# Kernel optimization log

Hardware: AMD Instinct MI355X
Metric: run time of the kernel (lower is better)

## Reference

```python
import jax, jax.numpy as jnp
import numpy as np

RES = 256
RADIUS = 1.3
N_INTRS = 128
STEP = 2.0 * RADIUS / N_INTRS
GRID_DIM = 2
RANK = 8


def bilinear_sample(grid, coords):
    """grid: [C,H,W]; coords: [N,2] in [-1,1] (x->W, y->H), align_corners=True, border clamp."""
    C, H, W = grid.shape
    x = jnp.clip((coords[:, 0] + 1.0) * 0.5 * (W - 1), 0.0, W - 1)
    y = jnp.clip((coords[:, 1] + 1.0) * 0.5 * (H - 1), 0.0, H - 1)
    x0 = jnp.clip(jnp.floor(x), 0, W - 2).astype(jnp.int32)
    y0 = jnp.clip(jnp.floor(y), 0, H - 2).astype(jnp.int32)
    x1, y1 = x0 + 1, y0 + 1
    wx = x - x0
    wy = y - y0
    g00 = grid[:, y0, x0]  # [C,N]
    g01 = grid[:, y0, x1]
    g10 = grid[:, y1, x0]
    g11 = grid[:, y1, x1]
    out = (g00 * (1 - wx) * (1 - wy) + g01 * wx * (1 - wy)
           + g10 * (1 - wx) * wy + g11 * wx * wy)
    return out.T  # [N,C]


def sh_deg4(d):
    """Spherical harmonics degree 4 (16 coeffs), d: [N,3] unit dirs."""
    x, y, z = d[:, 0], d[:, 1], d[:, 2]
    xx, yy, zz = x * x, y * y, z * z
    xy, yz, xz = x * y, y * z, x * z
    return jnp.stack([
        jnp.full_like(x, 0.28209479177387814),
        -0.48860251190291987 * y,
        0.48860251190291987 * z,
        -0.48860251190291987 * x,
        1.0925484305920792 * xy,
        -1.0925484305920792 * yz,
        0.94617469575755997 * zz - 0.31539156525251999,
        -1.0925484305920792 * xz,
        0.54627421529603959 * (xx - yy),
        0.59004358992664352 * y * (-3.0 * xx + yy),
        2.8906114426405538 * xy * z,
        0.45704579946446572 * y * (1.0 - 5.0 * zz),
        0.3731763325901154 * z * (5.0 * zz - 3.0),
        0.45704579946446572 * x * (1.0 - 5.0 * zz),
        1.445305721320277 * z * (xx - yy),
        0.59004358992664352 * x * (-xx + 3.0 * yy),
    ], axis=-1)  # [N,16]


def setup_inputs() -> dict:
    key = jax.random.key(0)
    ks = jax.random.split(key, 9)
    B = 16384
    # ray origins inside the sphere so every ray hits; random unit directions
    rays_o = jax.random.normal(ks[0], (B, 3), jnp.float32) * 0.3
    rays_d = jax.random.normal(ks[1], (B, 3), jnp.float32)
    G = jax.random.normal(ks[2], (3, GRID_DIM * RANK, RES, RES), jnp.float32) * 0.1
    Fgrid = jax.random.normal(ks[3], (32, 64, 64), jnp.float32) * 0.05
    sigma_W1 = jax.random.normal(ks[4], (32, 64), jnp.float32) * (1.0 / np.sqrt(32))
    sigma_W2 = jax.random.normal(ks[5], (64, 16), jnp.float32) * (1.0 / np.sqrt(64))
    color_W1 = jax.random.normal(ks[6], (31, 64), jnp.float32) * (1.0 / np.sqrt(31))
    color_W2 = jax.random.normal(ks[7], (64, 64), jnp.float32) * (1.0 / np.sqrt(64))
    color_W3 = jax.random.normal(ks[8], (64, 3), jnp.float32) * (1.0 / np.sqrt(64))
    return {"rays_o": rays_o, "rays_d": rays_d, "G": G, "Fgrid": Fgrid,
            "sigma_W1": sigma_W1, "sigma_W2": sigma_W2,
            "color_W1": color_W1, "color_W2": color_W2, "color_W3": color_W3}


def reference(rays_o, rays_d, G, Fgrid, sigma_W1, sigma_W2, color_W1, color_W2, color_W3):
    B = rays_o.shape[0]
    d = rays_d / jnp.linalg.norm(rays_d, axis=-1, keepdims=True)
    # ray-sphere intersection (|o + t d| = RADIUS), d unit
    b = jnp.sum(rays_o * d, axis=-1)
    c = jnp.sum(rays_o * rays_o, axis=-1) - RADIUS ** 2
    disc = b * b - c
    sq = jnp.sqrt(jnp.maximum(disc, 0.0))
    near = jnp.maximum(-b - sq, 0.0)
    far = -b + sq
    ts = near[:, None] + jnp.arange(N_INTRS + 1, dtype=jnp.float32) * STEP  # [B, n+1]
    tmid = 0.5 * (ts[:, :-1] + ts[:, 1:])  # [B, n]
    mask = (disc > 0)[:, None] & (tmid <= far[:, None])  # [B, n]
    pts = rays_o[:, None, :] + d[:, None, :] * tmid[..., None]  # [B, n, 3]
    # combined rescale: ((pts/R + 1)*RES/2) * 2/RES - 1 = pts / RADIUS
    p = (pts / RADIUS).reshape(-1, 3)  # [N, 3] in ~[-1,1]
    # tri-plane sampling
    coo = jnp.stack([p[:, [0, 1]], p[:, [0, 2]], p[:, [1, 2]]])  # [3, N, 2]
    interp = jax.vmap(bilinear_sample)(G, coo)  # [3, N, GRID_DIM*RANK]
    interp = interp.reshape(3, -1, GRID_DIM, RANK)
    Gvals = interp.prod(axis=0).sum(axis=-1)  # [N, GRID_DIM]
    Fvals = bilinear_sample(Fgrid, Gvals)  # [N, feature_dim]
    h = jax.nn.relu(Fvals @ sigma_W1) @ sigma_W2  # [N, 16]
    sigma_pts = h[:, 0]
    feat = h[:, 1:]
    rd = jnp.broadcast_to(d[:, None, :], (B, N_INTRS, 3)).reshape(-1, 3)
    enc = sh_deg4(rd)  # [N, 16]
    cin = jnp.concatenate([enc, feat], axis=-1)  # [N, 31]
    col = jax.nn.relu(jax.nn.relu(cin @ color_W1) @ color_W2) @ color_W3  # [N, 3]
    mflat = mask.reshape(-1)
    sigma = jax.nn.relu(jnp.where(mflat, sigma_pts, 0.0)).reshape(B, N_INTRS)
    color = jnp.where(mflat[:, None], col, 0.0).reshape(B, N_INTRS, 3)
    # sigma2alpha + compositing (white background)
    delta = ts[:, 1:] - ts[:, :-1]
    alpha = 1.0 - jnp.exp(-sigma * delta)
    trans = jnp.cumprod(1.0 - alpha + 1e-10, axis=1)
    T = jnp.concatenate([jnp.ones_like(trans[:, :1]), trans[:, :-1]], axis=1)
    w = alpha * T  # [B, n]
    rgb = jax.nn.sigmoid(color)
    acc = jnp.sum(w, axis=1)
    out = jnp.einsum('bn,bnc->bc', w, rgb) + (1.0 - acc)[:, None]
    return out
```

## Files before the change

kernel.cpp:

```cpp
#include <hip/hip_runtime.h>
#include <math.h>

#define B_RAYS 16384
#define N_I 128
constexpr float RADIUS_ = 1.3f;
constexpr float STEP_ = 0.0203125f;

typedef float v2f __attribute__((ext_vector_type(2)));
static __device__ __forceinline__ v2f mk2(float a, float b) { v2f r; r.x = a; r.y = b; return r; }
static __device__ __forceinline__ v2f vfma(v2f a, v2f b, v2f c) {
    return __builtin_elementwise_fma(a, b, c);
}

__global__ __launch_bounds__(256) void k_transposeG(const float* __restrict__ G,
                                                    float* __restrict__ Gt) {
    int pl = blockIdx.x >> 8;
    int y  = blockIdx.x & 255;
    __shared__ float tile[16][257];
    int t = threadIdx.x;
#pragma unroll
    for (int ch = 0; ch < 16; ++ch)
        tile[ch][t] = G[((pl * 16 + ch) * 256 + y) * 256 + t];
    __syncthreads();
    float* dst = Gt + (pl * 256 + y) * 256 * 16;
#pragma unroll
    for (int i = 0; i < 16; ++i) {
        int o = i * 256 + t;
        dst[o] = tile[o & 15][o >> 4];
    }
}

__global__ __launch_bounds__(256) void k_transposeF(const float* __restrict__ F,
                                                    float* __restrict__ Ft) {
    int y = blockIdx.x;
    __shared__ float tile[32][65];
    int t = threadIdx.x;
#pragma unroll
    for (int i = 0; i < 8; ++i) {
        int o = i * 256 + t;
        tile[o >> 6][o & 63] = F[((o >> 6) * 64 + y) * 64 + (o & 63)];
    }
    __syncthreads();
    float* dst = Ft + y * 64 * 32;
#pragma unroll
    for (int i = 0; i < 8; ++i) {
        int o = i * 256 + t;
        dst[o] = tile[o & 31][o >> 5];
    }
}

__global__ __launch_bounds__(256) void k_fused(
    const float* __restrict__ rays_o, const float* __restrict__ rays_d,
    const float* __restrict__ Gt, const float* __restrict__ Ft,
    const float* __restrict__ sW1, const float* __restrict__ sW2,
    const float* __restrict__ cW1, const float* __restrict__ cW2,
    const float* __restrict__ cW3, float* __restrict__ out) {
    __shared__ float w_s1t[64 * 32];
    __shared__ float w_s2[64 * 16];
    __shared__ float w_c1t[64 * 32];
    __shared__ float w_c2[64 * 64];
    __shared__ float w_c3[64 * 3];
    int tid = threadIdx.x;
    for (int i = tid; i < 2048; i += 256) { float v = sW1[i]; w_s1t[(i & 63) * 32 + (i >> 6)] = v; }
    for (int i = tid; i < 1024; i += 256) w_s2[i] = sW2[i];
    for (int i = tid; i < 1984; i += 256) { float v = cW1[i]; w_c1t[(i & 63) * 32 + (i >> 6)] = v; }
    for (int i = tid; i < 64; i += 256) w_c1t[i * 32 + 31] = 0.f;
    for (int i = tid; i < 4096; i += 256) w_c2[i] = cW2[i];
    if (tid < 192) w_c3[tid] = cW3[tid];
    __syncthreads();

    int lane = tid & 63;
    int ray  = (blockIdx.x << 2) + (tid >> 6);

    float ox = rays_o[ray * 3 + 0], oy = rays_o[ray * 3 + 1], oz = rays_o[ray * 3 + 2];
    float rx = rays_d[ray * 3 + 0], ry = rays_d[ray * 3 + 1], rz = rays_d[ray * 3 + 2];
    float nrm = sqrtf(rx * rx + ry * ry + rz * rz);
    float dx = rx / nrm, dy = ry / nrm, dz = rz / nrm;
    float bq = ox * dx + oy * dy + oz * dz;
    float cq = ox * ox + oy * oy + oz * oz - RADIUS_ * RADIUS_;
    float disc = bq * bq - cq;
    float sq = sqrtf(fmaxf(disc, 0.f));
    float tnear = fmaxf(-bq - sq, 0.f);
    float tfar = -bq + sq;

    v2f e[8];
    {
        float x = dx, y = dy, z = dz;
        float xx = x * x, yy = y * y, zz = z * z;
        float xy = x * y, yz = y * z, xz = x * z;
        e[0] = mk2(0.28209479177387814f, -0.48860251190291987f * y);
        e[1] = mk2(0.48860251190291987f * z, -0.48860251190291987f * x);
        e[2] = mk2(1.0925484305920792f * xy, -1.0925484305920792f * yz);
        e[3] = mk2(0.94617469575756f * zz - 0.31539156525252f, -1.0925484305920792f * xz);
        e[4] = mk2(0.5462742152960396f * (xx - yy),
                   0.5900435899266435f * y * (-3.0f * xx + yy));
        e[5] = mk2(2.890611442640554f * xy * z,
                   0.4570457994644657f * y * (1.0f - 5.0f * zz));
        e[6] = mk2(0.3731763325901154f * z * (5.0f * zz - 3.0f),
                   0.4570457994644657f * x * (1.0f - 5.0f * zz));
        e[7] = mk2(1.445305721320277f * z * (xx - yy),
                   0.5900435899266435f * x * (-xx + 3.0f * yy));
    }

    float4 res[2];
#pragma unroll
    for (int u = 0; u < 2; ++u) {
        int s = (lane << 1) + u;
        float t0 = tnear + (float)s * STEP_;
        float t1 = tnear + (float)(s + 1) * STEP_;
        float tmid = 0.5f * (t0 + t1);
        bool mask = (disc > 0.f) && (tmid <= tfar);
        if (!mask) {
            res[u] = make_float4(0.f, 0.f, 0.f, 0.f);
        } else {
            float px = (ox + dx * tmid) / RADIUS_;
            float py = (oy + dy * tmid) / RADIUS_;
            float pz = (oz + dz * tmid) / RADIUS_;

            v2f pr[8];
            float cxs[3] = {px, px, py};
            float cys[3] = {py, pz, pz};
#pragma unroll
            for (int pl = 0; pl < 3; ++pl) {
                float fx = fminf(fmaxf((cxs[pl] + 1.0f) * 0.5f * 255.0f, 0.f), 255.f);
                float fy = fminf(fmaxf((cys[pl] + 1.0f) * 0.5f * 255.0f, 0.f), 255.f);
                float x0f = fminf(floorf(fx), 254.f);
                float y0f = fminf(floorf(fy), 254.f);
                int x0 = (int)x0f, y0 = (int)y0f;
                float wx = fx - x0f, wy = fy - y0f;
                v2f w00 = mk2((1.f - wx) * (1.f - wy), (1.f - wx) * (1.f - wy));
                v2f w01 = mk2(wx * (1.f - wy), wx * (1.f - wy));
                v2f w10 = mk2((1.f - wx) * wy, (1.f - wx) * wy);
                v2f w11 = mk2(wx * wy, wx * wy);
                const float* b00 = Gt + ((pl * 256 + y0) * 256 + x0) * 16;
#pragma unroll
                for (int q = 0; q < 4; ++q) {
                    float4 g00 = *(const float4*)(b00 + q * 4);
                    float4 g01 = *(const float4*)(b00 + 16 + q * 4);
                    float4 g10 = *(const float4*)(b00 + 4096 + q * 4);
                    float4 g11 = *(const float4*)(b00 + 4112 + q * 4);
                    v2f lo = mk2(g00.x, g00.y) * w00;
                    lo = vfma(mk2(g01.x, g01.y), w01, lo);
                    lo = vfma(mk2(g10.x, g10.y), w10, lo);
                    lo = vfma(mk2(g11.x, g11.y), w11, lo);
                    v2f hi = mk2(g00.z, g00.w) * w00;
                    hi = vfma(mk2(g01.z, g01.w), w01, hi);
                    hi = vfma(mk2(g10.z, g10.w), w10, hi);
                    hi = vfma(mk2(g11.z, g11.w), w11, hi);
                    if (pl == 0) { pr[2 * q] = lo; pr[2 * q + 1] = hi; }
                    else         { pr[2 * q] *= lo; pr[2 * q + 1] *= hi; }
                }
            }
            v2f sx = (pr[0] + pr[1]) + (pr[2] + pr[3]);
            v2f sy = (pr[4] + pr[5]) + (pr[6] + pr[7]);
            float Gx = sx.x + sx.y;
            float Gy = sy.x + sy.y;

            v2f fv[16];
            {
                float fx = fminf(fmaxf((Gx + 1.0f) * 0.5f * 63.0f, 0.f), 63.f);
                float fy = fminf(fmaxf((Gy + 1.0f) * 0.5f * 63.0f, 0.f), 63.f);
                float x0f = fminf(floorf(fx), 62.f);
                float y0f = fminf(floorf(fy), 62.f);
                int x0 = (int)x0f, y0 = (int)y0f;
                float wx = fx - x0f, wy = fy - y0f;
                v2f w00 = mk2((1.f - wx) * (1.f - wy), (1.f - wx) * (1.f - wy));
                v2f w01 = mk2(wx * (1.f - wy), wx * (1.f - wy));
                v2f w10 = mk2((1.f - wx) * wy, (1.f - wx) * wy);
                v2f w11 = mk2(wx * wy, wx * wy);
                const float* f00 = Ft + (y0 * 64 + x0) * 32;
#pragma unroll
                for (int q = 0; q < 8; ++q) {
                    float4 g00 = *(const float4*)(f00 + q * 4);
                    float4 g01 = *(const float4*)(f00 + 32 + q * 4);
                    float4 g10 = *(const float4*)(f00 + 2048 + q * 4);
                    float4 g11 = *(const float4*)(f00 + 2048 + 32 + q * 4);
                    v2f lo = mk2(g00.x, g00.y) * w00;
                    lo = vfma(mk2(g01.x, g01.y), w01, lo);
                    lo = vfma(mk2(g10.x, g10.y), w10, lo);
                    lo = vfma(mk2(g11.x, g11.y), w11, lo);
                    v2f hi = mk2(g00.z, g00.w) * w00;
                    hi = vfma(mk2(g01.z, g01.w), w01, hi);
                    hi = vfma(mk2(g10.z, g10.w), w10, hi);
                    hi = vfma(mk2(g11.z, g11.w), w11, hi);
                    fv[2 * q] = lo;
                    fv[2 * q + 1] = hi;
                }
            }

            v2f hh2[8];
#pragma unroll
            for (int m = 0; m < 8; ++m) hh2[m] = mk2(0.f, 0.f);
            for (int j = 0; j < 64; ++j) {
                const float4* wrow = (const float4*)&w_s1t[j * 32];
                v2f aA = mk2(0.f, 0.f), aB = mk2(0.f, 0.f);
#pragma unroll
                for (int q = 0; q < 8; ++q) {
                    float4 w = wrow[q];
                    aA = vfma(fv[2 * q], mk2(w.x, w.y), aA);
                    aB = vfma(fv[2 * q + 1], mk2(w.z, w.w), aB);
                }
                v2f asum = aA + aB;
                float a = fmaxf(asum.x + asum.y, 0.f);
                v2f av = mk2(a, a);
                const float4* w2row = (const float4*)&w_s2[j * 16];
#pragma unroll
                for (int q = 0; q < 4; ++q) {
                    float4 w = w2row[q];
                    hh2[2 * q] = vfma(av, mk2(w.x, w.y), hh2[2 * q]);
                    hh2[2 * q + 1] = vfma(av, mk2(w.z, w.w), hh2[2 * q + 1]);
                }
            }

            v2f cf[8];
            cf[0] = mk2(hh2[0].y, hh2[1].x);
            cf[1] = mk2(hh2[1].y, hh2[2].x);
            cf[2] = mk2(hh2[2].y, hh2[3].x);
            cf[3] = mk2(hh2[3].y, hh2[4].x);
            cf[4] = mk2(hh2[4].y, hh2[5].x);
            cf[5] = mk2(hh2[5].y, hh2[6].x);
            cf[6] = mk2(hh2[6].y, hh2[7].x);
            cf[7] = mk2(hh2[7].y, 0.f);

            v2f c2v[32];
#pragma unroll
            for (int m = 0; m < 32; ++m) c2v[m] = mk2(0.f, 0.f);
            for (int j = 0; j < 64; ++j) {
                const float4* wrow = (const float4*)&w_c1t[j * 32];
                v2f aA = mk2(0.f, 0.f), aB = mk2(0.f, 0.f);
#pragma unroll
                for (int q = 0; q < 4; ++q) {
                    float4 w = wrow[q];
                    aA = vfma(e[2 * q], mk2(w.x, w.y), aA);
                    aB = vfma(e[2 * q + 1], mk2(w.z, w.w), aB);
                }
#pragma unroll
                for (int q = 0; q < 4; ++q) {
                    float4 w = wrow[4 + q];
                    aA = vfma(cf[2 * q], mk2(w.x, w.y), aA);
                    aB = vfma(cf[2 * q + 1], mk2(w.z, w.w), aB);
                }
                v2f asum = aA + aB;
                float a = fmaxf(asum.x + asum.y, 0.f);
                v2f av = mk2(a, a);
                const float4* w2row = (const float4*)&w_c2[j * 64];
#pragma unroll
                for (int q = 0; q < 16; ++q) {
                    float4 w = w2row[q];
                    c2v[2 * q] = vfma(av, mk2(w.x, w.y), c2v[2 * q]);
                    c2v[2 * q + 1] = vfma(av, mk2(w.z, w.w), c2v[2 * q + 1]);
                }
            }
            v2f col01 = mk2(0.f, 0.f);
            float col2 = 0.f;
#pragma unroll
            for (int m = 0; m < 64; ++m) {
                float v = fmaxf((m & 1) ? c2v[m >> 1].y : c2v[m >> 1].x, 0.f);
                col01 = vfma(mk2(v, v), mk2(w_c3[m * 3 + 0], w_c3[m * 3 + 1]), col01);
                col2 = fmaf(v, w_c3[m * 3 + 2], col2);
            }

            float sigma = fmaxf(hh2[0].x, 0.f);
            float r = 1.f / (1.f + expf(-col01.x));
            float g = 1.f / (1.f + expf(-col01.y));
            float b = 1.f / (1.f + expf(-col2));
            res[u] = make_float4(sigma, r, g, b);
        }
    }

    int s0 = lane * 2;
    float4 p0 = res[0];
    float4 p1 = res[1];
    float ta = tnear + (float)s0 * STEP_;
    float tb = tnear + (float)(s0 + 1) * STEP_;
    float tc = tnear + (float)(s0 + 2) * STEP_;
    float d0 = tb - ta, d1 = tc - tb;
    float alpha0 = 1.f - expf(-p0.x * d0);
    float alpha1 = 1.f - expf(-p1.x * d1);
    float f0 = (1.f - alpha0) + 1e-10f;
    float f1 = (1.f - alpha1) + 1e-10f;
    float fp = f0 * f1;

    float P = fp;
#pragma unroll
    for (int dlt = 1; dlt < 64; dlt <<= 1) {
        float v = __shfl_up(P, dlt, 64);
        if (lane >= dlt) P *= v;
    }
    float E = __shfl_up(P, 1, 64);
    if (lane == 0) E = 1.f;

    float w0 = alpha0 * E;
    float w1 = alpha1 * (E * f0);
    float sr = w0 * p0.y + w1 * p1.y;
    float sg = w0 * p0.z + w1 * p1.z;
    float sb = w0 * p0.w + w1 * p1.w;
    float sa = w0 + w1;
#pragma unroll
    for (int m = 32; m >= 1; m >>= 1) {
        sr += __shfl_xor(sr, m, 64);
        sg += __shfl_xor(sg, m, 64);
        sb += __shfl_xor(sb, m, 64);
        sa += __shfl_xor(sa, m, 64);
    }
    if (lane == 0) {
        float bg = 1.f - sa;
        out[ray * 3 + 0] = sr + bg;
        out[ray * 3 + 1] = sg + bg;
        out[ray * 3 + 2] = sb + bg;
    }
}

extern "C" void kernel_launch(void* const* d_in, const int* in_sizes, int n_in,
                              void* d_out, int out_size, void* d_ws, size_t ws_size,
                              hipStream_t stream) {
    const float* rays_o = (const float*)d_in[0];
    const float* rays_d = (const float*)d_in[1];
    const float* G      = (const float*)d_in[2];
    const float* Fgrid  = (const float*)d_in[3];
    const float* sW1    = (const float*)d_in[4];
    const float* sW2    = (const float*)d_in[5];
    const float* cW1    = (const float*)d_in[6];
    const float* cW2    = (const float*)d_in[7];
    const float* cW3    = (const float*)d_in[8];
    float* out = (float*)d_out;

    char* ws = (char*)d_ws;
    float* Gt = (float*)ws;
    float* Ft = (float*)(ws + 12582912);

    k_transposeG<<<768, 256, 0, stream>>>(G, Gt);
    k_transposeF<<<64, 256, 0, stream>>>(Fgrid, Ft);
    k_fused<<<B_RAYS / 4, 256, 0, stream>>>(
        rays_o, rays_d, Gt, Ft, sW1, sW2, cW1, cW2, cW3, out);
}
```

Measured before the change: 824.3 us.

## Process two samples per lane jointly to share LDS weight loads

Restructures the per-lane loop so both samples of a lane run through the triplane gather, feature gather and both MLPs together, sharing each LDS weight row read across two samples. It also transposes the final color weights for float4 LDS reads and adds a waves-per-EU hint. This raises register pressure (two 64-wide accumulators at once) and may spill or lower occupancy. When sample A is active, sample B's MLP is computed and then discarded if it is masked.

After: 804.1 us. 2.4% less time.

```diff
diff --git a/kernel.cpp b/kernel.cpp
--- a/kernel.cpp
+++ b/kernel.cpp
@@ -49,7 +49,79 @@
     }
 }
 
-__global__ __launch_bounds__(256) void k_fused(
+#define FGRID_GATHER(GXQ, GYQ, FVOUT)                                              \
+    {                                                                              \
+        float fx = fminf(fmaxf(((GXQ) + 1.0f) * 0.5f * 63.0f, 0.f), 63.f);         \
+        float fy = fminf(fmaxf(((GYQ) + 1.0f) * 0.5f * 63.0f, 0.f), 63.f);         \
+        float x0f = fminf(floorf(fx), 62.f);                                       \
+        float y0f = fminf(floorf(fy), 62.f);                                       \
+        int x0 = (int)x0f, y0 = (int)y0f;                                          \
+        float wx = fx - x0f, wy = fy - y0f;                                        \
+        v2f w00 = mk2((1.f - wx) * (1.f - wy), (1.f - wx) * (1.f - wy));           \
+        v2f w01 = mk2(wx * (1.f - wy), wx * (1.f - wy));                           \
+        v2f w10 = mk2((1.f - wx) * wy, (1.f - wx) * wy);                           \
+        v2f w11 = mk2(wx * wy, wx * wy);                                           \
+        const float* f00 = Ft + (y0 * 64 + x0) * 32;                               \
+        _Pragma("unroll") for (int q = 0; q < 8; ++q) {                            \
+            float4 g00 = *(const float4*)(f00 + q * 4);                            \
+            float4 g01 = *(const float4*)(f00 + 32 + q * 4);                       \
+            float4 g10 = *(const float4*)(f00 + 2048 + q * 4);                     \
+            float4 g11 = *(const float4*)(f00 + 2048 + 32 + q * 4);                \
+            v2f lo = mk2(g00.x, g00.y) * w00;                                      \
+            lo = vfma(mk2(g01.x, g01.y), w01, lo);                                 \
+            lo = vfma(mk2(g10.x, g10.y), w10, lo);                                 \
+            lo = vfma(mk2(g11.x, g11.y), w11, lo);                                 \
+            v2f hi = mk2(g00.z, g00.w) * w00;                                      \
+            hi = vfma(mk2(g01.z, g01.w), w01, hi);                                 \
+            hi = vfma(mk2(g10.z, g10.w), w10, hi);                                 \
+            hi = vfma(mk2(g11.z, g11.w), w11, hi);                                 \
+            FVOUT[2 * q] = lo;                                                     \
+            FVOUT[2 * q + 1] = hi;                                                 \
+        }                                                                          \
+    }
+
+#define TRIPLANE(PX, PY, PZ, GXOUT, GYOUT)                                         \
+    {                                                                              \
+        v2f pr[8];                                                                 \
+        float cxs[3] = {(PX), (PX), (PY)};                                         \
+        float cys[3] = {(PY), (PZ), (PZ)};                                         \
+        _Pragma("unroll") for (int pl = 0; pl < 3; ++pl) {                         \
+            float fx = fminf(fmaxf((cxs[pl] + 1.0f) * 0.5f * 255.0f, 0.f), 255.f); \
+            float fy = fminf(fmaxf((cys[pl] + 1.0f) * 0.5f * 255.0f, 0.f), 255.f); \
+            float x0f = fminf(floorf(fx), 254.f);                                  \
+            float y0f = fminf(floorf(fy), 254.f);                                  \
+            int x0 = (int)x0f, y0 = (int)y0f;                                      \
+            float wx = fx - x0f, wy = fy - y0f;                                    \
+            v2f w00 = mk2((1.f - wx) * (1.f - wy), (1.f - wx) * (1.f - wy));       \
+            v2f w01 = mk2(wx * (1.f - wy), wx * (1.f - wy));                       \
+            v2f w10 = mk2((1.f - wx) * wy, (1.f - wx) * wy);                       \
+            v2f w11 = mk2(wx * wy, wx * wy);                                       \
+            const float* b00 = Gt + ((pl * 256 + y0) * 256 + x0) * 16;             \
+            _Pragma("unroll") for (int q = 0; q < 4; ++q) {                        \
+                float4 g00 = *(const float4*)(b00 + q * 4);                        \
+                float4 g01 = *(const float4*)(b00 + 16 + q * 4);                   \
+                float4 g10 = *(const float4*)(b00 + 4096 + q * 4);                 \
+                float4 g11 = *(const float4*)(b00 + 4112 + q * 4);                 \
+                v2f lo = mk2(g00.x, g00.y) * w00;                                  \
+                lo = vfma(mk2(g01.x, g01.y), w01, lo);                             \
+                lo = vfma(mk2(g10.x, g10.y), w10, lo);                             \
+                lo = vfma(mk2(g11.x, g11.y), w11, lo);                             \
+                v2f hi = mk2(g00.z, g00.w) * w00;                                  \
+                hi = vfma(mk2(g01.z, g01.w), w01, hi);                             \
+                hi = vfma(mk2(g10.z, g10.w), w10, hi);                             \
+                hi = vfma(mk2(g11.z, g11.w), w11, hi);                             \
+                if (pl == 0) { pr[2 * q] = lo; pr[2 * q + 1] = hi; }               \
+                else         { pr[2 * q] *= lo; pr[2 * q + 1] *= hi; }             \
+            }                                                                      \
+        }                                                                          \
+        v2f sx = (pr[0] + pr[1]) + (pr[2] + pr[3]);                                \
+        v2f sy = (pr[4] + pr[5]) + (pr[6] + pr[7]);                                \
+        GXOUT = sx.x + sx.y;                                                       \
+        GYOUT = sy.x + sy.y;                                                       \
+    }
+
+__global__ void __launch_bounds__(256)
+    __attribute__((amdgpu_waves_per_eu(2, 4))) k_fused(
     const float* __restrict__ rays_o, const float* __restrict__ rays_d,
     const float* __restrict__ Gt, const float* __restrict__ Ft,
     const float* __restrict__ sW1, const float* __restrict__ sW2,
@@ -59,14 +131,14 @@
     __shared__ float w_s2[64 * 16];
     __shared__ float w_c1t[64 * 32];
     __shared__ float w_c2[64 * 64];
-    __shared__ float w_c3[64 * 3];
+    __shared__ float w_c3t[3 * 64];
     int tid = threadIdx.x;
     for (int i = tid; i < 2048; i += 256) { float v = sW1[i]; w_s1t[(i & 63) * 32 + (i >> 6)] = v; }
     for (int i = tid; i < 1024; i += 256) w_s2[i] = sW2[i];
     for (int i = tid; i < 1984; i += 256) { float v = cW1[i]; w_c1t[(i & 63) * 32 + (i >> 6)] = v; }
     for (int i = tid; i < 64; i += 256) w_c1t[i * 32 + 31] = 0.f;
     for (int i = tid; i < 4096; i += 256) w_c2[i] = cW2[i];
-    if (tid < 192) w_c3[tid] = cW3[tid];
+    if (tid < 192) w_c3t[(tid % 3) * 64 + tid / 3] = cW3[tid];
     __syncthreads();
 
     int lane = tid & 63;
@@ -102,181 +174,172 @@
                    0.5900435899266435f * x * (-xx + 3.0f * yy));
     }
 
-    float4 res[2];
-#pragma unroll
-    for (int u = 0; u < 2; ++u) {
-        int s = (lane << 1) + u;
-        float t0 = tnear + (float)s * STEP_;
-        float t1 = tnear + (float)(s + 1) * STEP_;
-        float tmid = 0.5f * (t0 + t1);
-        bool mask = (disc > 0.f) && (tmid <= tfar);
-        if (!mask) {
-            res[u] = make_float4(0.f, 0.f, 0.f, 0.f);
-        } else {
-            float px = (ox + dx * tmid) / RADIUS_;
-            float py = (oy + dy * tmid) / RADIUS_;
-            float pz = (oz + dz * tmid) / RADIUS_;
-
-            v2f pr[8];
-            float cxs[3] = {px, px, py};
-            float cys[3] = {py, pz, pz};
-#pragma unroll
-            for (int pl = 0; pl < 3; ++pl) {
-                float fx = fminf(fmaxf((cxs[pl] + 1.0f) * 0.5f * 255.0f, 0.f), 255.f);
-                float fy = fminf(fmaxf((cys[pl] + 1.0f) * 0.5f * 255.0f, 0.f), 255.f);
-                float x0f = fminf(floorf(fx), 254.f);
-                float y0f = fminf(floorf(fy), 254.f);
-                int x0 = (int)x0f, y0 = (int)y0f;
-                float wx = fx - x0f, wy = fy - y0f;
-                v2f w00 = mk2((1.f - wx) * (1.f - wy), (1.f - wx) * (1.f - wy));
-                v2f w01 = mk2(wx * (1.f - wy), wx * (1.f - wy));
-                v2f w10 = mk2((1.f - wx) * wy, (1.f - wx) * wy);
-                v2f w11 = mk2(wx * wy, wx * wy);
-                const float* b00 = Gt + ((pl * 256 + y0) * 256 + x0) * 16;
-#pragma unroll
-                for (int q = 0; q < 4; ++q) {
-                    float4 g00 = *(const float4*)(b00 + q * 4);
-                    float4 g01 = *(const float4*)(b00 + 16 + q * 4);
-                    float4 g10 = *(const float4*)(b00 + 4096 + q * 4);
-                    float4 g11 = *(const float4*)(b00 + 4112 + q * 4);
-                    v2f lo = mk2(g00.x, g00.y) * w00;
-                    lo = vfma(mk2(g01.x, g01.y), w01, lo);
-                    lo = vfma(mk2(g10.x, g10.y), w10, lo);
-                    lo = vfma(mk2(g11.x, g11.y), w11, lo);
-                    v2f hi = mk2(g00.z, g00.w) * w00;
-                    hi = vfma(mk2(g01.z, g01.w), w01, hi);
-                    hi = vfma(mk2(g10.z, g10.w), w10, hi);
-                    hi = vfma(mk2(g11.z, g11.w), w11, hi);
-                    if (pl == 0) { pr[2 * q] = lo; pr[2 * q + 1] = hi; }
-                    else         { pr[2 * q] *= lo; pr[2 * q + 1] *= hi; }
-                }
-            }
-            v2f sx = (pr[0] + pr[1]) + (pr[2] + pr[3]);
-            v2f sy = (pr[4] + pr[5]) + (pr[6] + pr[7]);
-            float Gx = sx.x + sx.y;
-            float Gy = sy.x + sy.y;
-
-            v2f fv[16];
-            {
-                float fx = fminf(fmaxf((Gx + 1.0f) * 0.5f * 63.0f, 0.f), 63.f);
-                float fy = fminf(fmaxf((Gy + 1.0f) * 0.5f * 63.0f, 0.f), 63.f);
-                float x0f = fminf(floorf(fx), 62.f);
-                float y0f = fminf(floorf(fy), 62.f);
-                int x0 = (int)x0f, y0 = (int)y0f;
-                float wx = fx - x0f, wy = fy - y0f;
-                v2f w00 = mk2((1.f - wx) * (1.f - wy), (1.f - wx) * (1.f - wy));
-                v2f w01 = mk2(wx * (1.f - wy), wx * (1.f - wy));
-                v2f w10 = mk2((1.f - wx) * wy, (1.f - wx) * wy);
-                v2f w11 = mk2(wx * wy, wx * wy);
-                const float* f00 = Ft + (y0 * 64 + x0) * 32;
-#pragma unroll
-                for (int q = 0; q < 8; ++q) {
-                    float4 g00 = *(const float4*)(f00 + q * 4);
-                    float4 g01 = *(const float4*)(f00 + 32 + q * 4);
-                    float4 g10 = *(const float4*)(f00 + 2048 + q * 4);
-                    float4 g11 = *(const float4*)(f00 + 2048 + 32 + q * 4);
-                    v2f lo = mk2(g00.x, g00.y) * w00;
-                    lo = vfma(mk2(g01.x, g01.y), w01, lo);
-                    lo = vfma(mk2(g10.x, g10.y), w10, lo);
-                    lo = vfma(mk2(g11.x, g11.y), w11, lo);
-                    v2f hi = mk2(g00.z, g00.w) * w00;
-                    hi = vfma(mk2(g01.z, g01.w), w01, hi);
-                    hi = vfma(mk2(g10.z, g10.w), w10, hi);
-                    hi = vfma(mk2(g11.z, g11.w), w11, hi);
-                    fv[2 * q] = lo;
-                    fv[2 * q + 1] = hi;
-                }
-            }
-
-            v2f hh2[8];
-#pragma unroll
-            for (int m = 0; m < 8; ++m) hh2[m] = mk2(0.f, 0.f);
-            for (int j = 0; j < 64; ++j) {
-                const float4* wrow = (const float4*)&w_s1t[j * 32];
-                v2f aA = mk2(0.f, 0.f), aB = mk2(0.f, 0.f);
-#pragma unroll
-                for (int q = 0; q < 8; ++q) {
-                    float4 w = wrow[q];
-                    aA = vfma(fv[2 * q], mk2(w.x, w.y), aA);
-                    aB = vfma(fv[2 * q + 1], mk2(w.z, w.w), aB);
-                }
-                v2f asum = aA + aB;
-                float a = fmaxf(asum.x + asum.y, 0.f);
-                v2f av = mk2(a, a);
-                const float4* w2row = (const float4*)&w_s2[j * 16];
-#pragma unroll
-                for (int q = 0; q < 4; ++q) {
-                    float4 w = w2row[q];
-                    hh2[2 * q] = vfma(av, mk2(w.x, w.y), hh2[2 * q]);
-                    hh2[2 * q + 1] = vfma(av, mk2(w.z, w.w), hh2[2 * q + 1]);
-                }
-            }
-
-            v2f cf[8];
-            cf[0] = mk2(hh2[0].y, hh2[1].x);
-            cf[1] = mk2(hh2[1].y, hh2[2].x);
-            cf[2] = mk2(hh2[2].y, hh2[3].x);
-            cf[3] = mk2(hh2[3].y, hh2[4].x);
-            cf[4] = mk2(hh2[4].y, hh2[5].x);
-            cf[5] = mk2(hh2[5].y, hh2[6].x);
-            cf[6] = mk2(hh2[6].y, hh2[7].x);
-            cf[7] = mk2(hh2[7].y, 0.f);
-
-            v2f c2v[32];
-#pragma unroll
-            for (int m = 0; m < 32; ++m) c2v[m] = mk2(0.f, 0.f);
-            for (int j = 0; j < 64; ++j) {
-                const float4* wrow = (const float4*)&w_c1t[j * 32];
-                v2f aA = mk2(0.f, 0.f), aB = mk2(0.f, 0.f);
-#pragma unroll
-                for (int q = 0; q < 4; ++q) {
-                    float4 w = wrow[q];
-                    aA = vfma(e[2 * q], mk2(w.x, w.y), aA);
-                    aB = vfma(e[2 * q + 1], mk2(w.z, w.w), aB);
-                }
-#pragma unroll
-                for (int q = 0; q < 4; ++q) {
-                    float4 w = wrow[4 + q];
-                    aA = vfma(cf[2 * q], mk2(w.x, w.y), aA);
-                    aB = vfma(cf[2 * q + 1], mk2(w.z, w.w), aB);
-                }
-                v2f asum = aA + aB;
-                float a = fmaxf(asum.x + asum.y, 0.f);
-                v2f av = mk2(a, a);
-                const float4* w2row = (const float4*)&w_c2[j * 64];
-#pragma unroll
-                for (int q = 0; q < 16; ++q) {
-                    float4 w = w2row[q];
-                    c2v[2 * q] = vfma(av, mk2(w.x, w.y), c2v[2 * q]);
-                    c2v[2 * q + 1] = vfma(av, mk2(w.z, w.w), c2v[2 * q + 1]);
-                }
-            }
-            v2f col01 = mk2(0.f, 0.f);
-            float col2 = 0.f;
-#pragma unroll
-            for (int m = 0; m < 64; ++m) {
-                float v = fmaxf((m & 1) ? c2v[m >> 1].y : c2v[m >> 1].x, 0.f);
-                col01 = vfma(mk2(v, v), mk2(w_c3[m * 3 + 0], w_c3[m * 3 + 1]), col01);
-                col2 = fmaf(v, w_c3[m * 3 + 2], col2);
-            }
-
-            float sigma = fmaxf(hh2[0].x, 0.f);
-            float r = 1.f / (1.f + expf(-col01.x));
-            float g = 1.f / (1.f + expf(-col01.y));
-            float b = 1.f / (1.f + expf(-col2));
-            res[u] = make_float4(sigma, r, g, b);
+    int sA = lane << 1;
+    float t0A = tnear + (float)sA * STEP_;
+    float t1A = tnear + (float)(sA + 1) * STEP_;
+    float t1B = tnear + (float)(sA + 2) * STEP_;
+    float tmidA = 0.5f * (t0A + t1A);
+    float tmidB = 0.5f * (t1A + t1B);
+    bool maskA = (disc > 0.f) && (tmidA <= tfar);
+    bool maskB = (disc > 0.f) && (tmidB <= tfar);
+
+    float4 resA = make_float4(0.f, 0.f, 0.f, 0.f);
+    float4 resB = make_float4(0.f, 0.f, 0.f, 0.f);
+
+    if (maskA) {
+        float pxA = (ox + dx * tmidA) / RADIUS_;
+        float pyA = (oy + dy * tmidA) / RADIUS_;
+        float pzA = (oz + dz * tmidA) / RADIUS_;
+        float pxB = (ox + dx * tmidB) / RADIUS_;
+        float pyB = (oy + dy * tmidB) / RADIUS_;
+        float pzB = (oz + dz * tmidB) / RADIUS_;
+
+        float GxA, GyA, GxB, GyB;
+        TRIPLANE(pxA, pyA, pzA, GxA, GyA);
+        TRIPLANE(pxB, pyB, pzB, GxB, GyB);
+
+        v2f fvA[16], fvB[16];
+        FGRID_GATHER(GxA, GyA, fvA);
+        FGRID_GATHER(GxB, GyB, fvB);
+
+        v2f hhA[8], hhB[8];
+#pragma unroll
+        for (int m = 0; m < 8; ++m) { hhA[m] = mk2(0.f, 0.f); hhB[m] = mk2(0.f, 0.f); }
+        for (int j = 0; j < 64; ++j) {
+            const float4* wrow = (const float4*)&w_s1t[j * 32];
+            v2f aA0 = mk2(0.f, 0.f), aB0 = mk2(0.f, 0.f);
+            v2f aA1 = mk2(0.f, 0.f), aB1 = mk2(0.f, 0.f);
+#pragma unroll
+            for (int q = 0; q < 8; ++q) {
+                float4 w = wrow[q];
+                v2f wlo = mk2(w.x, w.y), whi = mk2(w.z, w.w);
+                aA0 = vfma(fvA[2 * q], wlo, aA0);
+                aB0 = vfma(fvA[2 * q + 1], whi, aB0);
+                aA1 = vfma(fvB[2 * q], wlo, aA1);
+                aB1 = vfma(fvB[2 * q + 1], whi, aB1);
+            }
+            v2f s0 = aA0 + aB0;
+            v2f s1 = aA1 + aB1;
+            float a0 = fmaxf(s0.x + s0.y, 0.f);
+            float a1 = fmaxf(s1.x + s1.y, 0.f);
+            v2f av0 = mk2(a0, a0), av1 = mk2(a1, a1);
+            const float4* w2row = (const float4*)&w_s2[j * 16];
+#pragma unroll
+            for (int q = 0; q < 4; ++q) {
+                float4 w = w2row[q];
+                v2f wlo = mk2(w.x, w.y), whi = mk2(w.z, w.w);
+                hhA[2 * q] = vfma(av0, wlo, hhA[2 * q]);
+                hhA[2 * q + 1] = vfma(av0, whi, hhA[2 * q + 1]);
+                hhB[2 * q] = vfma(av1, wlo, hhB[2 * q]);
+                hhB[2 * q + 1] = vfma(av1, whi, hhB[2 * q + 1]);
+            }
         }
-    }
-
-    int s0 = lane * 2;
-    float4 p0 = res[0];
-    float4 p1 = res[1];
-    float ta = tnear + (float)s0 * STEP_;
-    float tb = tnear + (float)(s0 + 1) * STEP_;
-    float tc = tnear + (float)(s0 + 2) * STEP_;
+
+        float sigmaA = fmaxf(hhA[0].x, 0.f);
+        float sigmaB = fmaxf(hhB[0].x, 0.f);
+
+        v2f cfA[8], cfB[8];
+        cfA[0] = mk2(hhA[0].y, hhA[1].x); cfB[0] = mk2(hhB[0].y, hhB[1].x);
+        cfA[1] = mk2(hhA[1].y, hhA[2].x); cfB[1] = mk2(hhB[1].y, hhB[2].x);
+        cfA[2] = mk2(hhA[2].y, hhA[3].x); cfB[2] = mk2(hhB[2].y, hhB[3].x);
+        cfA[3] = mk2(hhA[3].y, hhA[4].x); cfB[3] = mk2(hhB[3].y, hhB[4].x);
+        cfA[4] = mk2(hhA[4].y, hhA[5].x); cfB[4] = mk2(hhB[4].y, hhB[5].x);
+        cfA[5] = mk2(hhA[5].y, hhA[6].x); cfB[5] = mk2(hhB[5].y, hhB[6].x);
+        cfA[6] = mk2(hhA[6].y, hhA[7].x); cfB[6] = mk2(hhB[6].y, hhB[7].x);
+        cfA[7] = mk2(hhA[7].y, 0.f);      cfB[7] = mk2(hhB[7].y, 0.f);
+
+        v2f c2A[32], c2B[32];
+#pragma unroll
+        for (int m = 0; m < 32; ++m) { c2A[m] = mk2(0.f, 0.f); c2B[m] = mk2(0.f, 0.f); }
+        for (int j = 0; j < 64; ++j) {
+            const float4* wrow = (const float4*)&w_c1t[j * 32];
+            v2f aA0 = mk2(0.f, 0.f), aB0 = mk2(0.f, 0.f);
+            v2f aA1 = mk2(0.f, 0.f), aB1 = mk2(0.f, 0.f);
+#pragma unroll
+            for (int q = 0; q < 4; ++q) {
+                float4 w = wrow[q];
+                v2f wlo = mk2(w.x, w.y), whi = mk2(w.z, w.w);
+                aA0 = vfma(e[2 * q], wlo, aA0);
+                aB0 = vfma(e[2 * q + 1], whi, aB0);
+                aA1 = vfma(e[2 * q], wlo, aA1);
+                aB1 = vfma(e[2 * q + 1], whi, aB1);
+            }
+#pragma unroll
+            for (int q = 0; q < 4; ++q) {
+                float4 w = wrow[4 + q];
+                v2f wlo = mk2(w.x, w.y), whi = mk2(w.z, w.w);
+                aA0 = vfma(cfA[2 * q], wlo, aA0);
+                aB0 = vfma(cfA[2 * q + 1], whi, aB0);
+                aA1 = vfma(cfB[2 * q], wlo, aA1);
+                aB1 = vfma(cfB[2 * q + 1], whi, aB1);
+            }
+            v2f s0 = aA0 + aB0;
+            v2f s1 = aA1 + aB1;
+            float a0 = fmaxf(s0.x + s0.y, 0.f);
+            float a1 = fmaxf(s1.x + s1.y, 0.f);
+            v2f av0 = mk2(a0, a0), av1 = mk2(a1, a1);
+            const float4* w2row = (const float4*)&w_c2[j * 64];
+#pragma unroll
+            for (int q = 0; q < 16; ++q) {
+                float4 w = w2row[q];
+                v2f wlo = mk2(w.x, w.y), whi = mk2(w.z, w.w);
+                c2A[2 * q] = vfma(av0, wlo, c2A[2 * q]);
+                c2A[2 * q + 1] = vfma(av0, whi, c2A[2 * q + 1]);
+                c2B[2 * q] = vfma(av1, wlo, c2B[2 * q]);
+                c2B[2 * q + 1] = vfma(av1, whi, c2B[2 * q + 1]);
+            }
+        }
+
+        v2f colA01 = mk2(0.f, 0.f), colB01 = mk2(0.f, 0.f);
+        float colA2 = 0.f, colB2 = 0.f;
+#pragma unroll
+        for (int mq = 0; mq < 16; ++mq) {
+            float4 wr = *(const float4*)&w_c3t[mq * 4];
+            float4 wg = *(const float4*)&w_c3t[64 + mq * 4];
+            float4 wb = *(const float4*)&w_c3t[128 + mq * 4];
+            v2f vaA = c2A[2 * mq], vbA = c2A[2 * mq + 1];
+            v2f vaB = c2B[2 * mq], vbB = c2B[2 * mq + 1];
+            float vA0 = fmaxf(vaA.x, 0.f), vA1 = fmaxf(vaA.y, 0.f);
+            float vA2 = fmaxf(vbA.x, 0.f), vA3 = fmaxf(vbA.y, 0.f);
+            float vB0 = fmaxf(vaB.x, 0.f), vB1 = fmaxf(vaB.y, 0.f);
+            float vB2 = fmaxf(vbB.x, 0.f), vB3 = fmaxf(vbB.y, 0.f);
+            colA01 = vfma(mk2(vA0, vA0), mk2(wr.x, wg.x), colA01);
+            colA01 = vfma(mk2(vA1, vA1), mk2(wr.y, wg.y), colA01);
+            colA01 = vfma(mk2(vA2, vA2), mk2(wr.z, wg.z), colA01);
+            colA01 = vfma(mk2(vA3, vA3), mk2(wr.w, wg.w), colA01);
+            colA2 = fmaf(vA0, wb.x, colA2);
+            colA2 = fmaf(vA1, wb.y, colA2);
+            colA2 = fmaf(vA2, wb.z, colA2);
+            colA2 = fmaf(vA3, wb.w, colA2);
+            colB01 = vfma(mk2(vB0, vB0), mk2(wr.x, wg.x), colB01);
+            colB01 = vfma(mk2(vB1, vB1), mk2(wr.y, wg.y), colB01);
+            colB01 = vfma(mk2(vB2, vB2), mk2(wr.z, wg.z), colB01);
+            colB01 = vfma(mk2(vB3, vB3), mk2(wr.w, wg.w), colB01);
+            colB2 = fmaf(vB0, wb.x, colB2);
+            colB2 = fmaf(vB1, wb.y, colB2);
+            colB2 = fmaf(vB2, wb.z, colB2);
+            colB2 = fmaf(vB3, wb.w, colB2);
+        }
+
+        resA = make_float4(sigmaA,
+                           1.f / (1.f + expf(-colA01.x)),
+                           1.f / (1.f + expf(-colA01.y)),
+                           1.f / (1.f + expf(-colA2)));
+        if (maskB) {
+            resB = make_float4(sigmaB,
+                               1.f / (1.f + expf(-colB01.x)),
+                               1.f / (1.f + expf(-colB01.y)),
+                               1.f / (1.f + expf(-colB2)));
+        }
+    }
+
+    int s0i = lane * 2;
+    float ta = tnear + (float)s0i * STEP_;
+    float tb = tnear + (float)(s0i + 1) * STEP_;
+    float tc = tnear + (float)(s0i + 2) * STEP_;
     float d0 = tb - ta, d1 = tc - tb;
-    float alpha0 = 1.f - expf(-p0.x * d0);
-    float alpha1 = 1.f - expf(-p1.x * d1);
+    float alpha0 = 1.f - expf(-resA.x * d0);
+    float alpha1 = 1.f - expf(-resB.x * d1);
     float f0 = (1.f - alpha0) + 1e-10f;
     float f1 = (1.f - alpha1) + 1e-10f;
     float fp = f0 * f1;
@@ -292,9 +355,9 @@
 
     float w0 = alpha0 * E;
     float w1 = alpha1 * (E * f0);
-    float sr = w0 * p0.y + w1 * p1.y;
-    float sg = w0 * p0.z + w1 * p1.z;
-    float sb = w0 * p0.w + w1 * p1.w;
+    float sr = w0 * resA.y + w1 * resB.y;
+    float sg = w0 * resA.z + w1 * resB.z;
+    float sb = w0 * resA.w + w1 * resB.w;
     float sa = w0 + w1;
 #pragma unroll
     for (int m = 32; m >= 1; m >>= 1) {
```
